# Optimization experiments

Measured on AMD Instinct MI355X. Metric: run time of the kernel, lower is better.

The kernel has to match this reference:

```python
import jax, jax.numpy as jnp
import numpy as np
import math

B, T, DM = 2, 2048, 2048
H, D = 16, 128
HALF = D // 2


def _rope_tables(T, half, base=10000.0):
    inv_freq = 1.0 / (base ** (np.arange(0, half, dtype=np.float32) / half))
    t = np.arange(T, dtype=np.float32)
    freqs = np.outer(t, inv_freq)  # [T, half]
    return jnp.asarray(np.cos(freqs)), jnp.asarray(np.sin(freqs))


def setup_inputs() -> dict:
    key = jax.random.key(0)
    ks = jax.random.split(key, 5)
    s = 1.0 / math.sqrt(DM)
    x = jax.random.normal(ks[0], (B, T, DM), dtype=jnp.float32)
    wq = jax.random.normal(ks[1], (H * D, DM), dtype=jnp.float32) * s
    wk = jax.random.normal(ks[2], (H * D, DM), dtype=jnp.float32) * s
    wv = jax.random.normal(ks[3], (H * D, DM), dtype=jnp.float32) * s
    wo = jax.random.normal(ks[4], (DM, H * D), dtype=jnp.float32) * s
    cos, sin = _rope_tables(T, HALF)
    return {"x": x, "wq": wq, "wk": wk, "wv": wv, "wo": wo, "cos": cos, "sin": sin}


def _apply_rope(x, cos, sin):
    # x: [B,H,T,D]; cos/sin: [T, D//2] broadcast over batch and head
    x1, x2 = x[..., :HALF], x[..., HALF:]
    c = cos[None, None]
    s = sin[None, None]
    return jnp.concatenate([x1 * c - x2 * s, x1 * s + x2 * c], axis=-1)


def reference(x, wq, wk, wv, wo, cos, sin):
    Bx, Tx, _ = x.shape
    # QKV projections (Linear with weight [out,in]): y = x @ W^T
    q = jnp.einsum('btd,ed->bte', x, wq).reshape(Bx, Tx, H, D).transpose(0, 2, 1, 3)
    k = jnp.einsum('btd,ed->bte', x, wk).reshape(Bx, Tx, H, D).transpose(0, 2, 1, 3)
    v = jnp.einsum('btd,ed->bte', x, wv).reshape(Bx, Tx, H, D).transpose(0, 2, 1, 3)
    q = _apply_rope(q, cos, sin)
    k = _apply_rope(k, cos, sin)
    # causal SDPA (prefill path: kv_cache=None, mask='causal')
    scale = 1.0 / math.sqrt(D)
    scores = jnp.einsum('bhqd,bhkd->bhqk', q, k) * scale  # [B,H,T,T]
    causal = jnp.tril(jnp.ones((Tx, Tx), dtype=bool))
    scores = jnp.where(causal[None, None], scores, jnp.finfo(scores.dtype).min)
    attn = jax.nn.softmax(scores, axis=-1)
    out = jnp.einsum('bhqk,bhkd->bhqd', attn, v)  # [B,H,T,D]
    out = out.transpose(0, 2, 1, 3).reshape(Bx, Tx, H * D)
    return jnp.einsum('bte,de->btd', out, wo)
```

## Files before the change

kernel.cpp:

```cpp
#include <hip/hip_runtime.h>

typedef __attribute__((ext_vector_type(8))) short short8;
typedef __attribute__((ext_vector_type(4))) float floatx4;

#define B_ 2
#define T_ 2048
#define DM_ 2048
#define H_ 16
#define D_ 128
#define HALF_ 64

__device__ inline unsigned short f2bf(float f) {
    union { float f; unsigned u; } v; v.f = f;
    unsigned r = (v.u + 0x7fffu + ((v.u >> 16) & 1u)) >> 16;
    return (unsigned short)r;
}

__device__ inline void gld16(const void* g, void* l) {
    __builtin_amdgcn_global_load_lds(
        (__attribute__((address_space(1))) void*)g,
        (__attribute__((address_space(3))) void*)l,
        16, 0, 0);
}

__global__ void conv_all(const float* __restrict__ x,
                         const float* __restrict__ w0, const float* __restrict__ w1,
                         const float* __restrict__ w2, const float* __restrict__ w3,
                         unsigned short* __restrict__ xb,
                         unsigned short* __restrict__ wb, int n4w) {
    int y = blockIdx.y;
    int i = blockIdx.x * 256 + threadIdx.x;
    const float* src;
    ushort4* dst;
    if (y < 2) { src = x + (size_t)y * n4w * 4; dst = (ushort4*)xb + (size_t)y * n4w; }
    else {
        src = (y == 2) ? w0 : (y == 3) ? w1 : (y == 4) ? w2 : w3;
        dst = (ushort4*)wb + (size_t)(y - 2) * n4w;
    }
    float4 f = ((const float4*)src)[i];
    ushort4 o;
    o.x = f2bf(f.x); o.y = f2bf(f.y); o.z = f2bf(f.z); o.w = f2bf(f.w);
    dst[i] = o;
}

__global__ __launch_bounds__(256)
void gemm_qkv(const unsigned short* __restrict__ A,
              const unsigned short* __restrict__ W,
              unsigned short* __restrict__ q,
              unsigned short* __restrict__ k,
              unsigned short* __restrict__ vt,
              const float* __restrict__ cosT,
              const float* __restrict__ sinT) {
    __shared__ unsigned short sh[18432];
    unsigned short* As = sh;
    unsigned short* Bs = sh + 4096;

    const int t    = threadIdx.x;
    const int lane = t & 63;
    const int w    = t >> 6;
    const int wm   = w >> 1, wn = w & 1;
    const int l15  = lane & 15, quad = lane >> 4;
    const int bx   = blockIdx.x;
    const int row0 = blockIdx.y * 128;
    const int colg0 = bx * 128;
    const int h     = bx & 15;
    const int K = DM_;

    floatx4 acc[4][4];
    for (int i = 0; i < 4; ++i)
        for (int j = 0; j < 4; ++j)
            acc[i][j] = (floatx4){0.f, 0.f, 0.f, 0.f};

    for (int kt = 0; kt < K / 32; ++kt) {
        if (kt) __syncthreads();
        for (int i = 0; i < 2; ++i) {
            int g  = i * 256 + t;
            int g0 = i * 256 + (t & ~63);
            int m  = g >> 2, c = g & 3;
            int k8 = c ^ ((m >> 1) & 3);
            gld16(A + (size_t)(row0 + m) * K + kt * 32 + k8 * 8, As + (size_t)g0 * 8);
            gld16(W + (size_t)(colg0 + m) * K + kt * 32 + k8 * 8, Bs + (size_t)g0 * 8);
        }
        __syncthreads();

        short8 a[4], b[4];
        for (int mf = 0; mf < 4; ++mf) {
            int row = wm * 64 + mf * 16 + l15;
            int pc  = quad ^ ((row >> 1) & 3);
            a[mf] = *(const short8*)(As + row * 32 + pc * 8);
        }
        for (int nf = 0; nf < 4; ++nf) {
            int row = wn * 32 + (nf & 1) * 16 + (nf >> 1) * 64 + l15;
            int pc  = quad ^ ((row >> 1) & 3);
            b[nf] = *(const short8*)(Bs + row * 32 + pc * 8);
        }
        for (int mf = 0; mf < 4; ++mf)
            for (int nf = 0; nf < 4; ++nf)
                acc[mf][nf] = __builtin_amdgcn_mfma_f32_16x16x32_bf16(
                    a[mf], b[nf], acc[mf][nf], 0, 0, 0);
    }

    if (bx < 32) {
        unsigned short* C = (bx < 16) ? q : k;
        for (int mf = 0; mf < 4; ++mf) {
            for (int nf = 0; nf < 2; ++nf) {
                int dh = wn * 32 + nf * 16 + l15;
                for (int r = 0; r < 4; ++r) {
                    int rowg = row0 + wm * 64 + mf * 16 + quad * 4 + r;
                    int tt = rowg & 2047;
                    float c = cosT[tt * 64 + dh];
                    float s = sinT[tt * 64 + dh];
                    float x1 = acc[mf][nf][r];
                    float x2 = acc[mf][nf + 2][r];
                    size_t base = (size_t)rowg * DM_ + h * D_ + dh;
                    C[base]         = f2bf(x1 * c - x2 * s);
                    C[base + HALF_] = f2bf(x1 * s + x2 * c);
                }
            }
        }
    } else {
        __syncthreads();
        unsigned short* P = sh + w * 4608;
        for (int mf = 0; mf < 4; ++mf)
            for (int nf = 0; nf < 4; ++nf) {
                int lc = nf * 16 + l15;
                ushort4 o4;
                o4.x = f2bf(acc[mf][nf][0]); o4.y = f2bf(acc[mf][nf][1]);
                o4.z = f2bf(acc[mf][nf][2]); o4.w = f2bf(acc[mf][nf][3]);
                *(ushort4*)(P + lc * 72 + mf * 16 + quad * 4) = o4;
            }
        __syncthreads();
        const int b  = row0 >> 11;
        const int t0 = (row0 & 2047) + wm * 64;
        for (int it = 0; it < 8; ++it) {
            int cidx = it * 64 + lane;
            int lc = cidx >> 3, t8 = cidx & 7;
            int dh = wn * 32 + ((lc >> 4) & 1) * 16 + (lc >> 5) * 64 + (lc & 15);
            uint4 d = *(const uint4*)(P + lc * 72 + t8 * 8);
            *(uint4*)(vt + ((size_t)(b * 16 + h) * 128 + dh) * T_ + t0 + t8 * 8) = d;
        }
    }
}

__global__ __launch_bounds__(256)
void gemm_bt(const unsigned short* __restrict__ A,
             const unsigned short* __restrict__ W,
             float* __restrict__ C, int M, int N, int K) {
    __shared__ unsigned short As[128 * 32];
    __shared__ unsigned short Bs[128 * 32];

    const int t    = threadIdx.x;
    const int lane = t & 63;
    const int w    = t >> 6;
    const int wm   = w >> 1, wn = w & 1;
    const int l15  = lane & 15, quad = lane >> 4;
    const int row0 = blockIdx.y * 128, col0 = blockIdx.x * 128;

    floatx4 acc[4][4];
    for (int i = 0; i < 4; ++i)
        for (int j = 0; j < 4; ++j)
            acc[i][j] = (floatx4){0.f, 0.f, 0.f, 0.f};

    const int nkt = K >> 5;
    for (int kt = 0; kt < nkt; ++kt) {
        if (kt) __syncthreads();
        for (int i = 0; i < 2; ++i) {
            int g  = i * 256 + t;
            int g0 = i * 256 + (t & ~63);
            int m  = g >> 2, c = g & 3;
            int k8 = c ^ ((m >> 1) & 3);
            gld16(A + (size_t)(row0 + m) * K + kt * 32 + k8 * 8,
                  (unsigned short*)As + (size_t)g0 * 8);
            gld16(W + (size_t)(col0 + m) * K + kt * 32 + k8 * 8,
                  (unsigned short*)Bs + (size_t)g0 * 8);
        }
        __syncthreads();

        short8 a[4], b[4];
        for (int mf = 0; mf < 4; ++mf) {
            int row = wm * 64 + mf * 16 + l15;
            int pc  = quad ^ ((row >> 1) & 3);
            a[mf] = *(const short8*)(As + row * 32 + pc * 8);
        }
        for (int nf = 0; nf < 4; ++nf) {
            int row = wn * 64 + nf * 16 + l15;
            int pc  = quad ^ ((row >> 1) & 3);
            b[nf] = *(const short8*)(Bs + row * 32 + pc * 8);
        }
        for (int mf = 0; mf < 4; ++mf)
            for (int nf = 0; nf < 4; ++nf)
                acc[mf][nf] = __builtin_amdgcn_mfma_f32_16x16x32_bf16(
                    a[mf], b[nf], acc[mf][nf], 0, 0, 0);
    }

    for (int mf = 0; mf < 4; ++mf)
        for (int nf = 0; nf < 4; ++nf)
            for (int r = 0; r < 4; ++r) {
                int row = row0 + wm * 64 + mf * 16 + quad * 4 + r;
                int col = col0 + wn * 64 + nf * 16 + l15;
                C[(size_t)row * N + col] = acc[mf][nf][r];
            }
}

__global__ __launch_bounds__(256)
void attn_kernel(const unsigned short* __restrict__ q,
                 const unsigned short* __restrict__ k,
                 const unsigned short* __restrict__ vt,
                 unsigned short* __restrict__ ao) {
    __shared__ unsigned short Ks[64 * 128];
    __shared__ unsigned short Vts[128 * 64];
    __shared__ unsigned short Pw[4][16 * 72];

    const int t    = threadIdx.x;
    const int lane = t & 63, w = t >> 6;
    const int l15  = lane & 15, quad = lane >> 4;
    const int qblk = (gridDim.x - 1) - blockIdx.x;
    const int bh   = blockIdx.y;
    const int b    = bh >> 4, h = bh & 15;
    const int qbase = qblk * 128;

    const size_t hoff  = (size_t)h * D_;
    const size_t bbase = (size_t)b * T_ * DM_;

    short8 qa[2][4];
    for (int rs = 0; rs < 2; ++rs) {
        const int qw = qbase + rs * 64 + w * 16;
        const unsigned short* qp = q + bbase + (size_t)(qw + l15) * DM_ + hoff + quad * 8;
        for (int ds = 0; ds < 4; ++ds)
            qa[rs][ds] = *(const short8*)(qp + ds * 32);
    }

    floatx4 o[2][8];
    float l_i[2][4];
    for (int rs = 0; rs < 2; ++rs) {
        for (int c = 0; c < 8; ++c) o[rs][c] = (floatx4){0.f, 0.f, 0.f, 0.f};
        for (int r = 0; r < 4; ++r) l_i[rs][r] = 0.f;
    }

    const float kS = 0.08838834764831845f;
    const int ktend = 2 * qblk + 1;

    for (int kt = 0; kt <= ktend; ++kt) {
        if (kt) __syncthreads();
        for (int i = 0; i < 4; ++i) {
            int it = w * 4 + i;
            int krow = it * 4 + (lane >> 4);
            int gck  = ((lane & 15) ^ (krow & 7));
            gld16(k + bbase + (size_t)(kt * 64 + krow) * DM_ + hoff + gck * 8,
                  (unsigned short*)Ks + it * 512);
            int vrow = it * 8 + (lane >> 3);
            int gcv  = ((lane & 7) ^ (vrow & 7));
            gld16(vt + ((size_t)bh * 128 + vrow) * T_ + kt * 64 + gcv * 8,
                  (unsigned short*)Vts + it * 512);
        }
        __syncthreads();

        for (int rs = 0; rs < 2; ++rs) {
            const int kd = 2 * qblk + rs;
            if (kt > kd) continue;
            const int qw = qbase + rs * 64 + w * 16;

            floatx4 s[4];
            for (int f = 0; f < 4; ++f) s[f] = (floatx4){0.f, 0.f, 0.f, 0.f};
            for (int ds = 0; ds < 4; ++ds)
                for (int f = 0; f < 4; ++f) {
                    int krow = f * 16 + l15;
                    int phys = (ds * 4 + quad) ^ (krow & 7);
                    short8 bf = *(const short8*)(Ks + krow * 128 + phys * 8);
                    s[f] = __builtin_amdgcn_mfma_f32_16x16x32_bf16(qa[rs][ds], bf, s[f], 0, 0, 0);
                }

            const bool diag = (kt == kd);
            for (int r = 0; r < 4; ++r) {
                int qrow = qw + quad * 4 + r;
                float p[4], sum = 0.f;
                for (int f = 0; f < 4; ++f) {
                    float x = s[f][r] * kS;
                    float e = __expf(x);
                    if (diag && (kt * 64 + f * 16 + l15 > qrow)) e = 0.f;
                    p[f] = e;
                    sum += e;
                }
                for (int off = 1; off < 16; off <<= 1)
                    sum += __shfl_xor(sum, off, 64);
                l_i[rs][r] += sum;
                for (int f = 0; f < 4; ++f)
                    Pw[w][(quad * 4 + r) * 72 + f * 16 + l15] = f2bf(p[f]);
            }

            short8 pa0 = *(const short8*)(&Pw[w][l15 * 72 + quad * 8]);
            short8 pa1 = *(const short8*)(&Pw[w][l15 * 72 + 32 + quad * 8]);
            for (int c = 0; c < 8; ++c) {
                int vrow = c * 16 + l15;
                short8 b0 = *(const short8*)(Vts + vrow * 64 + ((quad) ^ (vrow & 7)) * 8);
                short8 b1 = *(const short8*)(Vts + vrow * 64 + ((4 + quad) ^ (vrow & 7)) * 8);
                o[rs][c] = __builtin_amdgcn_mfma_f32_16x16x32_bf16(pa0, b0, o[rs][c], 0, 0, 0);
                o[rs][c] = __builtin_amdgcn_mfma_f32_16x16x32_bf16(pa1, b1, o[rs][c], 0, 0, 0);
            }
        }
    }

    for (int rs = 0; rs < 2; ++rs) {
        const int qw = qbase + rs * 64 + w * 16;
        for (int r = 0; r < 4; ++r) {
            float inv = 1.0f / l_i[rs][r];
            int qrow = qw + quad * 4 + r;
            size_t obase = bbase + (size_t)qrow * DM_ + hoff;
            for (int c = 0; c < 8; ++c)
                ao[obase + c * 16 + l15] = f2bf(o[rs][c][r] * inv);
        }
    }
}

extern "C" void kernel_launch(void* const* d_in, const int* in_sizes, int n_in,
                              void* d_out, int out_size, void* d_ws, size_t ws_size,
                              hipStream_t stream) {
    const float* x    = (const float*)d_in[0];
    const float* wq   = (const float*)d_in[1];
    const float* wk   = (const float*)d_in[2];
    const float* wv   = (const float*)d_in[3];
    const float* wo   = (const float*)d_in[4];
    const float* cosT = (const float*)d_in[5];
    const float* sinT = (const float*)d_in[6];
    float* out = (float*)d_out;

    const size_t NX = (size_t)B_ * T_ * DM_;
    const size_t NW = (size_t)DM_ * DM_;

    unsigned short* xb  = (unsigned short*)d_ws;
    unsigned short* wqb = xb + NX;
    unsigned short* wob = wqb + 3 * NW;
    unsigned short* qb  = wob + NW;
    unsigned short* kb  = qb + NX;
    unsigned short* vtb = kb + NX;
    unsigned short* aob = vtb + NX;

    conv_all<<<dim3((int)(NW / 4 / 256), 6), 256, 0, stream>>>(
        x, wq, wk, wv, wo, xb, wqb, (int)(NW / 4));

    gemm_qkv<<<dim3(48, 32), 256, 0, stream>>>(xb, wqb, qb, kb, vtb, cosT, sinT);

    attn_kernel<<<dim3(T_ / 128, B_ * H_), 256, 0, stream>>>(qb, kb, vtb, aob);

    gemm_bt<<<dim3(16, 32), 256, 0, stream>>>(aob, wob, out, B_ * T_, DM_, DM_);
}
```

Measured before the change: 428.3 us.

## Pair mirrored query tiles per block and compute row sums via MFMA

Each attention block now handles query tile 31-j together with tile j rather than two adjacent tiles, so every block does about the same amount of causal work. The per-row softmax denominator is now an MFMA of the bf16 probability tile against a ones vector, which removes the cross-lane shuffle reduction. This adds two MFMAs per tile and sums the bf16-rounded probabilities, which keeps the normaliser consistent with what P·V actually uses.

```diff
diff --git a/kernel.cpp b/kernel.cpp
--- a/kernel.cpp
+++ b/kernel.cpp
@@ -214,31 +214,34 @@
     const int t    = threadIdx.x;
     const int lane = t & 63, w = t >> 6;
     const int l15  = lane & 15, quad = lane >> 4;
-    const int qblk = (gridDim.x - 1) - blockIdx.x;
+    const int j    = blockIdx.x;
     const int bh   = blockIdx.y;
     const int b    = bh >> 4, h = bh & 15;
-    const int qbase = qblk * 128;
+    const int qt[2] = {31 - j, j};
 
     const size_t hoff  = (size_t)h * D_;
     const size_t bbase = (size_t)b * T_ * DM_;
 
     short8 qa[2][4];
     for (int rs = 0; rs < 2; ++rs) {
-        const int qw = qbase + rs * 64 + w * 16;
+        const int qw = qt[rs] * 64 + w * 16;
         const unsigned short* qp = q + bbase + (size_t)(qw + l15) * DM_ + hoff + quad * 8;
         for (int ds = 0; ds < 4; ++ds)
             qa[rs][ds] = *(const short8*)(qp + ds * 32);
     }
 
     floatx4 o[2][8];
-    float l_i[2][4];
+    floatx4 lacc[2];
     for (int rs = 0; rs < 2; ++rs) {
         for (int c = 0; c < 8; ++c) o[rs][c] = (floatx4){0.f, 0.f, 0.f, 0.f};
-        for (int r = 0; r < 4; ++r) l_i[rs][r] = 0.f;
-    }
+        lacc[rs] = (floatx4){0.f, 0.f, 0.f, 0.f};
+    }
+    const unsigned short one_bf = 0x3F80;
+    short8 ones;
+    for (int i = 0; i < 8; ++i) ones[i] = (short)one_bf;
 
     const float kS = 0.08838834764831845f;
-    const int ktend = 2 * qblk + 1;
+    const int ktend = qt[0];
 
     for (int kt = 0; kt <= ktend; ++kt) {
         if (kt) __syncthreads();
@@ -256,9 +259,9 @@
         __syncthreads();
 
         for (int rs = 0; rs < 2; ++rs) {
-            const int kd = 2 * qblk + rs;
+            const int kd = qt[rs];
             if (kt > kd) continue;
-            const int qw = qbase + rs * 64 + w * 16;
+            const int qw = qt[rs] * 64 + w * 16;
 
             floatx4 s[4];
             for (int f = 0; f < 4; ++f) s[f] = (floatx4){0.f, 0.f, 0.f, 0.f};
@@ -273,23 +276,18 @@
             const bool diag = (kt == kd);
             for (int r = 0; r < 4; ++r) {
                 int qrow = qw + quad * 4 + r;
-                float p[4], sum = 0.f;
                 for (int f = 0; f < 4; ++f) {
                     float x = s[f][r] * kS;
                     float e = __expf(x);
                     if (diag && (kt * 64 + f * 16 + l15 > qrow)) e = 0.f;
-                    p[f] = e;
-                    sum += e;
+                    Pw[w][(quad * 4 + r) * 72 + f * 16 + l15] = f2bf(e);
                 }
-                for (int off = 1; off < 16; off <<= 1)
-                    sum += __shfl_xor(sum, off, 64);
-                l_i[rs][r] += sum;
-                for (int f = 0; f < 4; ++f)
-                    Pw[w][(quad * 4 + r) * 72 + f * 16 + l15] = f2bf(p[f]);
             }
 
             short8 pa0 = *(const short8*)(&Pw[w][l15 * 72 + quad * 8]);
             short8 pa1 = *(const short8*)(&Pw[w][l15 * 72 + 32 + quad * 8]);
+            lacc[rs] = __builtin_amdgcn_mfma_f32_16x16x32_bf16(pa0, ones, lacc[rs], 0, 0, 0);
+            lacc[rs] = __builtin_amdgcn_mfma_f32_16x16x32_bf16(pa1, ones, lacc[rs], 0, 0, 0);
             for (int c = 0; c < 8; ++c) {
                 int vrow = c * 16 + l15;
                 short8 b0 = *(const short8*)(Vts + vrow * 64 + ((quad) ^ (vrow & 7)) * 8);
@@ -301,9 +299,9 @@
     }
 
     for (int rs = 0; rs < 2; ++rs) {
-        const int qw = qbase + rs * 64 + w * 16;
+        const int qw = qt[rs] * 64 + w * 16;
         for (int r = 0; r < 4; ++r) {
-            float inv = 1.0f / l_i[rs][r];
+            float inv = 1.0f / lacc[rs][r];
             int qrow = qw + quad * 4 + r;
             size_t obase = bbase + (size_t)qrow * DM_ + hoff;
             for (int c = 0; c < 8; ++c)
@@ -340,7 +338,7 @@
 
     gemm_qkv<<<dim3(48, 32), 256, 0, stream>>>(xb, wqb, qb, kb, vtb, cosT, sinT);
 
-    attn_kernel<<<dim3(T_ / 128, B_ * H_), 256, 0, stream>>>(qb, kb, vtb, aob);
+    attn_kernel<<<dim3(16, B_ * H_), 256, 0, stream>>>(qb, kb, vtb, aob);
 
     gemm_bt<<<dim3(16, 32), 256, 0, stream>>>(aob, wob, out, B_ * T_, DM_, DM_);
 }
```

After: 376.4 us. -12.1%, faster.
